# Performance work log

Hardware: AMD Instinct MI355X
Metric: run time of the kernel (lower is better)

The kernel has to match this reference:

```python
import jax, jax.numpy as jnp
import numpy as np

EMBED_DIM = 1024
NUM_HEAD = 16
HEAD_DIM = EMBED_DIM // NUM_HEAD
B, T = 4, 2048


def setup_inputs() -> dict:
    key = jax.random.key(0)
    ks = jax.random.split(key, 6)
    s_in = 1.0 / np.sqrt(EMBED_DIM)
    return {
        "hidden_states": jax.random.normal(ks[0], (B, T, EMBED_DIM), dtype=jnp.float32),
        "attn_mask": jnp.ones((B, T), dtype=jnp.int32),
        "W_qkv": jax.random.uniform(ks[1], (3 * EMBED_DIM, EMBED_DIM), jnp.float32, -s_in, s_in),
        "b_qkv": jax.random.uniform(ks[2], (3 * EMBED_DIM,), jnp.float32, -s_in, s_in),
        "W_o": jax.random.uniform(ks[3], (EMBED_DIM, EMBED_DIM), jnp.float32, -s_in, s_in),
        "b_o": jax.random.uniform(ks[4], (EMBED_DIM,), jnp.float32, -s_in, s_in),
    }


def reference(hidden_states, attn_mask, W_qkv, b_qkv, W_o, b_o):
    Bb, Tt, C = hidden_states.shape
    H, D = NUM_HEAD, HEAD_DIM
    scaling = D ** (-0.5)

    qkv = hidden_states @ W_qkv.T + b_qkv  # [B,T,3C]
    q, k, v = jnp.split(qkv, 3, axis=-1)
    # [B,H,T,D]
    q = q.reshape(Bb, Tt, H, D).transpose(0, 2, 1, 3)
    k = k.reshape(Bb, Tt, H, D).transpose(0, 2, 1, 3)
    v = v.reshape(Bb, Tt, H, D).transpose(0, 2, 1, 3)

    scores = jnp.einsum("bhqd,bhkd->bhqk", q, k) * scaling  # [B,H,T,T]

    causal = jnp.tril(jnp.ones((Tt, Tt), dtype=bool))[None, None]  # [1,1,T,T]
    am = attn_mask.astype(bool)
    mask = causal & am[:, None, :, None] & am[:, None, None, :]  # [B,1,T,T]
    scores = jnp.where(mask, scores, -jnp.inf)

    probs = jax.nn.softmax(scores, axis=-1)
    out = jnp.einsum("bhqk,bhkd->bhqd", probs, v)  # [B,H,T,D]
    out = out.transpose(0, 2, 1, 3).reshape(Bb, Tt, C)
    return out @ W_o.T + b_o
```

## Files before the change

kernel.cpp:

```cpp
#include <hip/hip_runtime.h>
#include <cstdint>
#include <cstddef>
#include <math.h>

#define BATCH 4
#define TSEQ  2048
#define CDIM  1024
#define NH    16
#define HDIM  64
#define MTOT  (BATCH * TSEQ)

typedef __attribute__((ext_vector_type(4))) float  floatx4;
typedef __attribute__((ext_vector_type(8))) short  shortx8;
typedef __attribute__((ext_vector_type(4))) short  shortx4;

__device__ __forceinline__ short f2bf(float f) {
    union { float f; unsigned int u; } v; v.f = f;
    unsigned int lsb = (v.u >> 16) & 1u;
    v.u += 0x7fffu + lsb;
    return (short)(v.u >> 16);
}

#if defined(__has_builtin)
#  if __has_builtin(__builtin_amdgcn_exp2f)
#    define EXP2F(x) __builtin_amdgcn_exp2f(x)
#  else
#    define EXP2F(x) exp2f(x)
#  endif
#  if __has_builtin(__builtin_amdgcn_perm)
__device__ __forceinline__ unsigned pack_hi16(unsigned hi, unsigned lo) {
    return __builtin_amdgcn_perm(hi, lo, 0x07060302u);
}
#  else
__device__ __forceinline__ unsigned pack_hi16(unsigned hi, unsigned lo) {
    return (lo >> 16) | (hi & 0xffff0000u);
}
#  endif
#  if __has_builtin(__builtin_amdgcn_mfma_f32_16x16x16bf16_1k)
#    define HAS_MFMA_1K 1
#  else
#    define HAS_MFMA_1K 0
#  endif
#else
#  define EXP2F(x) exp2f(x)
__device__ __forceinline__ unsigned pack_hi16(unsigned hi, unsigned lo) {
    return (lo >> 16) | (hi & 0xffff0000u);
}
#  define HAS_MFMA_1K 0
#endif

#define QSCALE (0.125f * 1.44269504088896f)

__global__ __launch_bounds__(256) void cvt_kernel(const float4* __restrict__ src,
                                                  shortx4* __restrict__ dst, int n4)
{
    int i = blockIdx.x * 256 + threadIdx.x;
    if (i < n4) {
        float4 v = src[i];
        shortx4 s;
        s[0] = f2bf(v.x); s[1] = f2bf(v.y); s[2] = f2bf(v.z); s[3] = f2bf(v.w);
        dst[i] = s;
    }
}

__global__ __launch_bounds__(256) void cvt3_kernel(
    const float4* __restrict__ s1, shortx4* __restrict__ d1,
    const float4* __restrict__ s2, shortx4* __restrict__ d2,
    const float4* __restrict__ s3, shortx4* __restrict__ d3)
{
    int bid = blockIdx.x;
    const float4* s; shortx4* d; int i;
    if (bid < 8192)       { s = s1; d = d1; i = bid * 256 + threadIdx.x; }
    else if (bid < 11264) { s = s2; d = d2; i = (bid - 8192) * 256 + threadIdx.x; }
    else                  { s = s3; d = d3; i = (bid - 11264) * 256 + threadIdx.x; }
    float4 v = s[i];
    shortx4 o;
    o[0] = f2bf(v.x); o[1] = f2bf(v.y); o[2] = f2bf(v.z); o[3] = f2bf(v.w);
    d[i] = o;
}

__device__ __forceinline__ void stageA_bf16(const short* g, short* S, int row0,
                                            int K, int k0, int tid, int wave)
{
#pragma unroll
    for (int i = 0; i < 2; ++i) {
        int c = i * 256 + tid;
        int r = c >> 2, kc = c & 3;
        __builtin_amdgcn_global_load_lds(
            (__attribute__((address_space(1))) void*)(g + (size_t)(row0 + r) * K + k0 + kc * 8),
            (__attribute__((address_space(3))) void*)((char*)S + i * 4096 + wave * 1024),
            16, 0, 0);
    }
}
__device__ __forceinline__ void stageB_f32(const float* g, short* S, int row0,
                                           int K, int k0, int tid)
{
#pragma unroll
    for (int i = 0; i < 4; ++i) {
        int c = i * 256 + tid;
        int r = c >> 3, fc = c & 7;
        const float4 v = *(const float4*)(g + (size_t)(row0 + r) * K + k0 + fc * 4);
        shortx4 s4;
        s4[0] = f2bf(v.x); s4[1] = f2bf(v.y); s4[2] = f2bf(v.z); s4[3] = f2bf(v.w);
        *(shortx4*)(S + r * 32 + fc * 4) = s4;
    }
}

__device__ __forceinline__ void qkv_epilogue(
    floatx4 (&acc)[4][4], const float* bias,
    short* Qo, short* Ko, short* VTo,
    int row0, int col0, int wr, int wc, int quad, int l16)
{
#pragma unroll
    for (int mi = 0; mi < 4; ++mi) {
        int m = row0 + wr * 64 + mi * 16 + quad * 4;
        int b = m >> 11, t0 = m & (TSEQ - 1);
#pragma unroll
        for (int ni = 0; ni < 4; ++ni) {
            int n = col0 + wc * 64 + ni * 16 + l16;
            float bv = bias[n];
            int part = n >> 10, rem = n & 1023;
            int h = rem >> 6, d = rem & 63;
            if (part == 2) {
                shortx4 st;
#pragma unroll
                for (int r = 0; r < 4; ++r) st[r] = f2bf(acc[mi][ni][r] + bv);
                *(shortx4*)(VTo + (((size_t)(b * NH + h)) * HDIM + d) * TSEQ + t0) = st;
            } else {
                short* dst = (part == 0) ? Qo : Ko;
                float scale = (part == 0) ? QSCALE : 1.0f;
#pragma unroll
                for (int r = 0; r < 4; ++r) {
                    size_t idx = (((size_t)(b * NH + h)) * TSEQ + (t0 + r)) * HDIM + d;
                    dst[idx] = f2bf((acc[mi][ni][r] + bv) * scale);
                }
            }
        }
    }
}

__global__ __launch_bounds__(256) void gemm_qkv_fast_kernel(
    const short* __restrict__ A,
    const short* __restrict__ W,
    const float* __restrict__ bias,
    short* __restrict__ Qo, short* __restrict__ Ko, short* __restrict__ VTo)
{
    __shared__ short As[128 * 32];
    __shared__ short Bs[128 * 32];
    const int tid  = threadIdx.x;
    const int lane = tid & 63, wave = tid >> 6;
    const int quad = lane >> 4, l16 = lane & 15;
    const int wr = wave >> 1, wc = wave & 1;
    const int row0 = blockIdx.x * 128;
    const int col0 = blockIdx.y * 128;
    const int K = CDIM;

    floatx4 acc[4][4] = {};

    for (int k0 = 0; k0 < K; k0 += 32) {
        stageA_bf16(A, As, row0, K, k0, tid, wave);
        stageA_bf16(W, Bs, col0, K, k0, tid, wave);
        __syncthreads();

        shortx8 af[4], bfr[4];
#pragma unroll
        for (int mi = 0; mi < 4; ++mi)
            af[mi] = *(const shortx8*)(As + (wr * 64 + mi * 16 + l16) * 32 + quad * 8);
#pragma unroll
        for (int ni = 0; ni < 4; ++ni)
            bfr[ni] = *(const shortx8*)(Bs + (wc * 64 + ni * 16 + l16) * 32 + quad * 8);
#pragma unroll
        for (int mi = 0; mi < 4; ++mi)
#pragma unroll
            for (int ni = 0; ni < 4; ++ni)
                acc[mi][ni] = __builtin_amdgcn_mfma_f32_16x16x32_bf16(
                    af[mi], bfr[ni], acc[mi][ni], 0, 0, 0);
        __syncthreads();
    }
    qkv_epilogue(acc, bias, Qo, Ko, VTo, row0, col0, wr, wc, quad, l16);
}

__global__ __launch_bounds__(256) void gemm_qkv_kernel(
    const short* __restrict__ A,
    const float* __restrict__ W,
    const float* __restrict__ bias,
    short* __restrict__ Qo, short* __restrict__ Ko, short* __restrict__ VTo)
{
    __shared__ short As[128 * 32];
    __shared__ short Bs[128 * 32];
    const int tid  = threadIdx.x;
    const int lane = tid & 63, wave = tid >> 6;
    const int quad = lane >> 4, l16 = lane & 15;
    const int wr = wave >> 1, wc = wave & 1;
    const int row0 = blockIdx.x * 128;
    const int col0 = blockIdx.y * 128;
    const int K = CDIM;

    floatx4 acc[4][4] = {};

    for (int k0 = 0; k0 < K; k0 += 32) {
        stageA_bf16(A, As, row0, K, k0, tid, wave);
        stageB_f32(W, Bs, col0, K, k0, tid);
        __syncthreads();

        shortx8 af[4], bfr[4];
#pragma unroll
        for (int mi = 0; mi < 4; ++mi)
            af[mi] = *(const shortx8*)(As + (wr * 64 + mi * 16 + l16) * 32 + quad * 8);
#pragma unroll
        for (int ni = 0; ni < 4; ++ni)
            bfr[ni] = *(const shortx8*)(Bs + (wc * 64 + ni * 16 + l16) * 32 + quad * 8);
#pragma unroll
        for (int mi = 0; mi < 4; ++mi)
#pragma unroll
            for (int ni = 0; ni < 4; ++ni)
                acc[mi][ni] = __builtin_amdgcn_mfma_f32_16x16x32_bf16(
                    af[mi], bfr[ni], acc[mi][ni], 0, 0, 0);
        __syncthreads();
    }
    qkv_epilogue(acc, bias, Qo, Ko, VTo, row0, col0, wr, wc, quad, l16);
}

__global__ __launch_bounds__(256) void attn_kernel(
    const short* __restrict__ Q,
    const short* __restrict__ Kg,
    const short* __restrict__ VT,
    const int*   __restrict__ am,
    short* __restrict__ O)
{
    __shared__ short Ks[64 * 64];
    __shared__ short Vs[64 * 64];

    const int tid  = threadIdx.x;
    const int lane = tid & 63, wave = tid >> 6;
    const int quad = lane >> 4, l16 = lane & 15;

    const int L = blockIdx.x;
    const int bh = (L & 7) + (((L >> 3) & 7) << 3);
    const int strip = 15 - (L >> 6);
    const int b = bh >> 4, h = bh & 15;

    const short* Qb = Q  + (size_t)bh * TSEQ * HDIM;
    const short* Kb = Kg + (size_t)bh * TSEQ * HDIM;
    const short* Vb = VT + (size_t)bh * HDIM * TSEQ;

    const int q0  = strip * 128;
    const int qb0 = q0 + wave * 32;
    const int qv0 = qb0 + l16;
    const int qv1 = qv0 + 16;

    shortx8 bq[2][2];
#pragma unroll
    for (int nq = 0; nq < 2; ++nq)
#pragma unroll
        for (int kk = 0; kk < 2; ++kk)
            bq[nq][kk] = *(const shortx8*)(
                Qb + (size_t)(qb0 + nq * 16 + l16) * HDIM + kk * 32 + quad * 8);

    floatx4 o[4][2] = {};
    floatx4 lacc[2] = {};

#if HAS_MFMA_1K
    const shortx4 ones4 = { (short)0x3F80, (short)0x3F80, (short)0x3F80, (short)0x3F80 };
#else
    const shortx8 ones8 = { (short)0x3F80, (short)0x3F80, (short)0x3F80, (short)0x3F80,
                            (short)0x3F80, (short)0x3F80, (short)0x3F80, (short)0x3F80 };
#endif

    const int ntiles = (q0 + 128) >> 6;
    for (int kt = 0; kt < ntiles; ++kt) {
        const int kt0 = kt << 6;
#pragma unroll
        for (int i = 0; i < 2; ++i) {
            int idx = i * 256 + tid;
            int rr = idx >> 3, cd = idx & 7;
            int c = cd ^ (rr & 7);
            __builtin_amdgcn_global_load_lds(
                (__attribute__((address_space(1))) void*)(Kb + (size_t)(kt0 + rr) * HDIM + c * 8),
                (__attribute__((address_space(3))) void*)((char*)Ks + i * 4096 + wave * 1024),
                16, 0, 0);
            __builtin_amdgcn_global_load_lds(
                (__attribute__((address_space(1))) void*)(Vb + (size_t)rr * TSEQ + kt0 + c * 8),
                (__attribute__((address_space(3))) void*)((char*)Vs + i * 4096 + wave * 1024),
                16, 0, 0);
        }
        int amv = am[b * TSEQ + kt0 + lane];
        bool allones = (__ballot(amv != 0) == 0xFFFFFFFFFFFFFFFFULL);
        __syncthreads();

        floatx4 s[4][2] = {};
#pragma unroll
        for (int kk = 0; kk < 2; ++kk)
#pragma unroll
            for (int t = 0; t < 4; ++t) {
                int rr = t * 16 + l16;
                shortx8 kf = *(const shortx8*)(
                    Ks + rr * 64 + (((kk * 4 + quad) ^ (l16 & 7)) << 3));
#pragma unroll
                for (int nq = 0; nq < 2; ++nq)
                    s[t][nq] = __builtin_amdgcn_mfma_f32_16x16x32_bf16(
                        kf, bq[nq][kk], s[t][nq], 0, 0, 0);
            }

        unsigned pk[4][2][2];
#pragma unroll
        for (int nq = 0; nq < 2; ++nq) {
            const int qv = nq ? qv1 : qv0;
#pragma unroll
            for (int t = 0; t < 4; ++t) {
                bool diag = (kt0 + t * 16 + 15) > (qb0 + nq * 16);
                unsigned pu[4];
#pragma unroll
                for (int r = 0; r < 4; ++r) {
                    float p = EXP2F(s[t][nq][r]);
                    unsigned u = __float_as_uint(p) & 0xffff0000u;
                    if (!allones) {
                        int amr = __shfl(amv, t * 16 + quad * 4 + r);
                        u = amr ? u : 0u;
                    }
                    if (diag) {
                        int kv = kt0 + t * 16 + quad * 4 + r;
                        u = (kv <= qv) ? u : 0u;
                    }
                    pu[r] = u;
                }
                pk[t][nq][0] = pack_hi16(pu[1], pu[0]);
                pk[t][nq][1] = pack_hi16(pu[3], pu[2]);
            }
        }

#if HAS_MFMA_1K
#pragma unroll
        for (int t = 0; t < 4; ++t) {
            union { unsigned u[2]; shortx4 s; } pb[2];
            pb[0].u[0] = pk[t][0][0]; pb[0].u[1] = pk[t][0][1];
            pb[1].u[0] = pk[t][1][0]; pb[1].u[1] = pk[t][1][1];
#pragma unroll
            for (int nq = 0; nq < 2; ++nq)
                lacc[nq] = __builtin_amdgcn_mfma_f32_16x16x16bf16_1k(
                    ones4, pb[nq].s, lacc[nq], 0, 0, 0);
#pragma unroll
            for (int mi = 0; mi < 4; ++mi) {
                int rr = mi * 16 + l16;
                int cidx = (2 * t + (quad >> 1)) ^ (l16 & 7);
                shortx4 vf = *(const shortx4*)(Vs + rr * 64 + cidx * 8 + (quad & 1) * 4);
#pragma unroll
                for (int nq = 0; nq < 2; ++nq)
                    o[mi][nq] = __builtin_amdgcn_mfma_f32_16x16x16bf16_1k(
                        vf, pb[nq].s, o[mi][nq], 0, 0, 0);
            }
        }
#else
#pragma unroll
        for (int kk2 = 0; kk2 < 2; ++kk2) {
            unsigned bfr[2][4];
#pragma unroll
            for (int nq = 0; nq < 2; ++nq)
#pragma unroll
                for (int jj = 0; jj < 4; ++jj) {
                    int srclane = (((quad & 1) * 2 + (jj >> 1)) * 16 + l16) << 2;
                    int lo = __builtin_amdgcn_ds_bpermute(srclane, (int)pk[kk2 * 2][nq][jj & 1]);
                    int hi = __builtin_amdgcn_ds_bpermute(srclane, (int)pk[kk2 * 2 + 1][nq][jj & 1]);
                    bfr[nq][jj] = (quad >> 1) ? (unsigned)hi : (unsigned)lo;
                }
            union { unsigned u[4]; shortx8 s; } pb[2];
#pragma unroll
            for (int nq = 0; nq < 2; ++nq) {
#pragma unroll
                for (int jj = 0; jj < 4; ++jj) pb[nq].u[jj] = bfr[nq][jj];
                lacc[nq] = __builtin_amdgcn_mfma_f32_16x16x32_bf16(
                    ones8, pb[nq].s, lacc[nq], 0, 0, 0);
            }
#pragma unroll
            for (int mi = 0; mi < 4; ++mi) {
                int rr = mi * 16 + l16;
                int cidx = (kk2 * 4 + quad) ^ (l16 & 7);
                shortx8 vf8 = *(const shortx8*)(Vs + rr * 64 + cidx * 8);
#pragma unroll
                for (int nq = 0; nq < 2; ++nq)
                    o[mi][nq] = __builtin_amdgcn_mfma_f32_16x16x32_bf16(
                        vf8, pb[nq].s, o[mi][nq], 0, 0, 0);
            }
        }
#endif
        __syncthreads();
    }

#pragma unroll
    for (int nq = 0; nq < 2; ++nq) {
        float inv = 1.0f / lacc[nq][0];
        int q = qb0 + nq * 16 + l16;
#pragma unroll
        for (int mi = 0; mi < 4; ++mi) {
            shortx4 st;
#pragma unroll
            for (int r = 0; r < 4; ++r) st[r] = f2bf(o[mi][nq][r] * inv);
            *(shortx4*)(O + ((size_t)(b * TSEQ + q)) * CDIM + h * HDIM + mi * 16 + quad * 4) = st;
        }
    }
}

__global__ __launch_bounds__(256) void gemm_out_kernel(
    const short* __restrict__ A,
    const short* __restrict__ W,
    const float* __restrict__ bias,
    float* __restrict__ Out)
{
    __shared__ short As[128 * 32];
    __shared__ short Bs[128 * 32];
    const int tid  = threadIdx.x;
    const int lane = tid & 63, wave = tid >> 6;
    const int quad = lane >> 4, l16 = lane & 15;
    const int wr = wave >> 1, wc = wave & 1;
    const int row0 = blockIdx.x * 128;
    const int col0 = blockIdx.y * 128;
    const int K = CDIM;

    floatx4 acc[4][4] = {};

    for (int k0 = 0; k0 < K; k0 += 32) {
        stageA_bf16(A, As, row0, K, k0, tid, wave);
        stageA_bf16(W, Bs, col0, K, k0, tid, wave);
        __syncthreads();

        shortx8 af[4], bfr[4];
#pragma unroll
        for (int mi = 0; mi < 4; ++mi)
            af[mi] = *(const shortx8*)(As + (wr * 64 + mi * 16 + l16) * 32 + quad * 8);
#pragma unroll
        for (int ni = 0; ni < 4; ++ni)
            bfr[ni] = *(const shortx8*)(Bs + (wc * 64 + ni * 16 + l16) * 32 + quad * 8);
#pragma unroll
        for (int mi = 0; mi < 4; ++mi)
#pragma unroll
            for (int ni = 0; ni < 4; ++ni)
                acc[mi][ni] = __builtin_amdgcn_mfma_f32_16x16x32_bf16(
                    af[mi], bfr[ni], acc[mi][ni], 0, 0, 0);
        __syncthreads();
    }

#pragma unroll
    for (int mi = 0; mi < 4; ++mi) {
        int m = row0 + wr * 64 + mi * 16 + quad * 4;
#pragma unroll
        for (int ni = 0; ni < 4; ++ni) {
            int n = col0 + wc * 64 + ni * 16 + l16;
            float bv = bias[n];
#pragma unroll
            for (int r = 0; r < 4; ++r)
                Out[(size_t)(m + r) * CDIM + n] = acc[mi][ni][r] + bv;
        }
    }
}

extern "C" void kernel_launch(void* const* d_in, const int* in_sizes, int n_in,
                              void* d_out, int out_size, void* d_ws, size_t ws_size,
                              hipStream_t stream)
{
    const float* hs   = (const float*)d_in[0];
    const int*   am   = (const int*)d_in[1];
    const float* Wqkv = (const float*)d_in[2];
    const float* bqkv = (const float*)d_in[3];
    const float* Wo   = (const float*)d_in[4];
    const float* bo   = (const float*)d_in[5];
    float* out = (float*)d_out;

    char* ws = (char*)d_ws;
    short* slot = (short*)ws;
    short* Qw   = (short*)(ws + ((size_t)16 << 20));
    short* Kw   = (short*)(ws + ((size_t)32 << 20));
    short* VTw  = (short*)(ws + ((size_t)48 << 20));

    if (ws_size >= ((size_t)72 << 20)) {
        short* Wqkvb = (short*)(ws + ((size_t)64 << 20));
        short* Wob   = (short*)(ws + ((size_t)70 << 20));
        cvt3_kernel<<<dim3(12288), 256, 0, stream>>>(
            (const float4*)hs,   (shortx4*)slot,
            (const float4*)Wqkv, (shortx4*)Wqkvb,
            (const float4*)Wo,   (shortx4*)Wob);
        gemm_qkv_fast_kernel<<<dim3(MTOT / 128, (3 * CDIM) / 128), 256, 0, stream>>>(
            slot, Wqkvb, bqkv, Qw, Kw, VTw);
        attn_kernel<<<dim3(1024), 256, 0, stream>>>(
            Qw, Kw, VTw, am, slot);
        gemm_out_kernel<<<dim3(MTOT / 128, CDIM / 128), 256, 0, stream>>>(
            slot, Wob, bo, out);
    } else {
        cvt_kernel<<<dim3((MTOT * CDIM / 4 + 255) / 256), 256, 0, stream>>>(
            (const float4*)hs, (shortx4*)slot, MTOT * CDIM / 4);
        gemm_qkv_kernel<<<dim3(MTOT / 128, (3 * CDIM) / 128), 256, 0, stream>>>(
            slot, Wqkv, bqkv, Qw, Kw, VTw);
        attn_kernel<<<dim3(1024), 256, 0, stream>>>(
            Qw, Kw, VTw, am, slot);
        cvt_kernel<<<dim3((CDIM * CDIM / 4 + 255) / 256), 256, 0, stream>>>(
            (const float4*)Wo, (shortx4*)Kw, CDIM * CDIM / 4);
        gemm_out_kernel<<<dim3(MTOT / 128, CDIM / 128), 256, 0, stream>>>(
            slot, Kw, bo, out);
    }
}
```

Before: 276.7 us.

## Double-buffer K/V tiles, skip fully masked causal subtiles, rebalance strip order

The attention kernel now double-buffers the K and V shared-memory tiles, so loading the next tile overlaps with computing the current one and each tile needs only one barrier. Each wave skips score and PV MFMAs for 16-key subtiles that lie entirely above its causal diagonal. Strip scheduling is reordered so long and short strips alternate across blocks. Launch bounds now request four blocks per CU. Doubling shared memory and adding the hint may increase register pressure or reduce occupancy.

```diff
diff --git a/kernel.cpp b/kernel.cpp
--- a/kernel.cpp
+++ b/kernel.cpp
@@ -221,23 +221,28 @@
     qkv_epilogue(acc, bias, Qo, Ko, VTo, row0, col0, wr, wc, quad, l16);
 }
 
-__global__ __launch_bounds__(256) void attn_kernel(
+__global__ __launch_bounds__(256, 4) void attn_kernel(
     const short* __restrict__ Q,
     const short* __restrict__ Kg,
     const short* __restrict__ VT,
     const int*   __restrict__ am,
     short* __restrict__ O)
 {
-    __shared__ short Ks[64 * 64];
-    __shared__ short Vs[64 * 64];
+    __shared__ short Ks[2 * 64 * 64];
+    __shared__ short Vs[2 * 64 * 64];
 
     const int tid  = threadIdx.x;
     const int lane = tid & 63, wave = tid >> 6;
     const int quad = lane >> 4, l16 = lane & 15;
 
     const int L = blockIdx.x;
-    const int bh = (L & 7) + (((L >> 3) & 7) << 3);
-    const int strip = 15 - (L >> 6);
+    const int bh = L & 63;
+    const int c  = L >> 6;
+    const int g  = c >> 2, ci = c & 3;
+    const int strip = (g == 0) ? (15 - ci)
+                    : (g == 1) ? ci
+                    : (g == 2) ? (8 + ci)
+                               : (7 - ci);
     const int b = bh >> 4, h = bh & 15;
 
     const short* Qb = Q  + (size_t)bh * TSEQ * HDIM;
@@ -248,6 +253,7 @@
     const int qb0 = q0 + wave * 32;
     const int qv0 = qb0 + l16;
     const int qv1 = qv0 + 16;
+    const int qmax = qb0 + 31;
 
     shortx8 bq[2][2];
 #pragma unroll
@@ -267,124 +273,153 @@
                             (short)0x3F80, (short)0x3F80, (short)0x3F80, (short)0x3F80 };
 #endif
 
+#define STAGE_KV(dstK, dstV, t0base)                                          \
+    {                                                                         \
+        _Pragma("unroll")                                                     \
+        for (int i = 0; i < 2; ++i) {                                         \
+            int idx = i * 256 + tid;                                          \
+            int rr = idx >> 3, cd = idx & 7;                                  \
+            int cc = cd ^ (rr & 7);                                           \
+            __builtin_amdgcn_global_load_lds(                                 \
+                (__attribute__((address_space(1))) void*)(Kb + (size_t)((t0base) + rr) * HDIM + cc * 8), \
+                (__attribute__((address_space(3))) void*)((char*)(dstK) + i * 4096 + wave * 1024),       \
+                16, 0, 0);                                                    \
+            __builtin_amdgcn_global_load_lds(                                 \
+                (__attribute__((address_space(1))) void*)(Vb + (size_t)rr * TSEQ + (t0base) + cc * 8),   \
+                (__attribute__((address_space(3))) void*)((char*)(dstV) + i * 4096 + wave * 1024),       \
+                16, 0, 0);                                                    \
+        }                                                                     \
+    }
+
     const int ntiles = (q0 + 128) >> 6;
+
+    STAGE_KV(Ks, Vs, 0);
+    __syncthreads();
+
     for (int kt = 0; kt < ntiles; ++kt) {
         const int kt0 = kt << 6;
-#pragma unroll
-        for (int i = 0; i < 2; ++i) {
-            int idx = i * 256 + tid;
-            int rr = idx >> 3, cd = idx & 7;
-            int c = cd ^ (rr & 7);
-            __builtin_amdgcn_global_load_lds(
-                (__attribute__((address_space(1))) void*)(Kb + (size_t)(kt0 + rr) * HDIM + c * 8),
-                (__attribute__((address_space(3))) void*)((char*)Ks + i * 4096 + wave * 1024),
-                16, 0, 0);
-            __builtin_amdgcn_global_load_lds(
-                (__attribute__((address_space(1))) void*)(Vb + (size_t)rr * TSEQ + kt0 + c * 8),
-                (__attribute__((address_space(3))) void*)((char*)Vs + i * 4096 + wave * 1024),
-                16, 0, 0);
+        const short* Kc = Ks + (kt & 1) * 4096;
+        const short* Vc = Vs + (kt & 1) * 4096;
+
+        if (kt + 1 < ntiles) {
+            short* Kn = Ks + ((kt + 1) & 1) * 4096;
+            short* Vn = Vs + ((kt + 1) & 1) * 4096;
+            const int nt0 = (kt + 1) << 6;
+            STAGE_KV(Kn, Vn, nt0);
         }
-        int amv = am[b * TSEQ + kt0 + lane];
-        bool allones = (__ballot(amv != 0) == 0xFFFFFFFFFFFFFFFFULL);
-        __syncthreads();
-
-        floatx4 s[4][2] = {};
-#pragma unroll
-        for (int kk = 0; kk < 2; ++kk)
+
+        if (kt0 <= qmax) {
+            int amv = am[b * TSEQ + kt0 + lane];
+            bool allones = (__ballot(amv != 0) == 0xFFFFFFFFFFFFFFFFULL);
+
+            floatx4 s[4][2] = {};
+#pragma unroll
+            for (int kk = 0; kk < 2; ++kk)
+#pragma unroll
+                for (int t = 0; t < 4; ++t) {
+                    if (kt0 + t * 16 > qmax) continue;
+                    int rr = t * 16 + l16;
+                    shortx8 kf = *(const shortx8*)(
+                        Kc + rr * 64 + (((kk * 4 + quad) ^ (l16 & 7)) << 3));
+#pragma unroll
+                    for (int nq = 0; nq < 2; ++nq)
+                        s[t][nq] = __builtin_amdgcn_mfma_f32_16x16x32_bf16(
+                            kf, bq[nq][kk], s[t][nq], 0, 0, 0);
+                }
+
+            unsigned pk[4][2][2];
+#pragma unroll
+            for (int nq = 0; nq < 2; ++nq) {
+                const int qv = nq ? qv1 : qv0;
+                const int qtop = qb0 + nq * 16 + 15;
+#pragma unroll
+                for (int t = 0; t < 4; ++t) {
+                    if (kt0 + t * 16 > qtop) {
+                        pk[t][nq][0] = 0u; pk[t][nq][1] = 0u;
+                        continue;
+                    }
+                    bool diag = (kt0 + t * 16 + 15) > (qb0 + nq * 16);
+                    unsigned pu[4];
+#pragma unroll
+                    for (int r = 0; r < 4; ++r) {
+                        float p = EXP2F(s[t][nq][r]);
+                        unsigned u = __float_as_uint(p);
+                        if (!allones) {
+                            int amr = __shfl(amv, t * 16 + quad * 4 + r);
+                            u = amr ? u : 0u;
+                        }
+                        if (diag) {
+                            int kv = kt0 + t * 16 + quad * 4 + r;
+                            u = (kv <= qv) ? u : 0u;
+                        }
+                        pu[r] = u;
+                    }
+                    pk[t][nq][0] = pack_hi16(pu[1], pu[0]);
+                    pk[t][nq][1] = pack_hi16(pu[3], pu[2]);
+                }
+            }
+
+#if HAS_MFMA_1K
 #pragma unroll
             for (int t = 0; t < 4; ++t) {
-                int rr = t * 16 + l16;
-                shortx8 kf = *(const shortx8*)(
-                    Ks + rr * 64 + (((kk * 4 + quad) ^ (l16 & 7)) << 3));
+                if (kt0 + t * 16 > qmax) continue;
+                union { unsigned u[2]; shortx4 s; } pb[2];
+                pb[0].u[0] = pk[t][0][0]; pb[0].u[1] = pk[t][0][1];
+                pb[1].u[0] = pk[t][1][0]; pb[1].u[1] = pk[t][1][1];
 #pragma unroll
                 for (int nq = 0; nq < 2; ++nq)
-                    s[t][nq] = __builtin_amdgcn_mfma_f32_16x16x32_bf16(
-                        kf, bq[nq][kk], s[t][nq], 0, 0, 0);
+                    lacc[nq] = __builtin_amdgcn_mfma_f32_16x16x16bf16_1k(
+                        ones4, pb[nq].s, lacc[nq], 0, 0, 0);
+#pragma unroll
+                for (int mi = 0; mi < 4; ++mi) {
+                    int rr = mi * 16 + l16;
+                    int cidx = (2 * t + (quad >> 1)) ^ (l16 & 7);
+                    shortx4 vf = *(const shortx4*)(Vc + rr * 64 + cidx * 8 + (quad & 1) * 4);
+#pragma unroll
+                    for (int nq = 0; nq < 2; ++nq)
+                        o[mi][nq] = __builtin_amdgcn_mfma_f32_16x16x16bf16_1k(
+                            vf, pb[nq].s, o[mi][nq], 0, 0, 0);
+                }
             }
-
-        unsigned pk[4][2][2];
-#pragma unroll
-        for (int nq = 0; nq < 2; ++nq) {
-            const int qv = nq ? qv1 : qv0;
-#pragma unroll
-            for (int t = 0; t < 4; ++t) {
-                bool diag = (kt0 + t * 16 + 15) > (qb0 + nq * 16);
-                unsigned pu[4];
-#pragma unroll
-                for (int r = 0; r < 4; ++r) {
-                    float p = EXP2F(s[t][nq][r]);
-                    unsigned u = __float_as_uint(p) & 0xffff0000u;
-                    if (!allones) {
-                        int amr = __shfl(amv, t * 16 + quad * 4 + r);
-                        u = amr ? u : 0u;
+#else
+#pragma unroll
+            for (int kk2 = 0; kk2 < 2; ++kk2) {
+                if (kt0 + kk2 * 32 > qmax) continue;
+                unsigned bfr[2][4];
+#pragma unroll
+                for (int nq = 0; nq < 2; ++nq)
+#pragma unroll
+                    for (int jj = 0; jj < 4; ++jj) {
+                        int srclane = (((quad & 1) * 2 + (jj >> 1)) * 16 + l16) << 2;
+                        int lo = __builtin_amdgcn_ds_bpermute(srclane, (int)pk[kk2 * 2][nq][jj & 1]);
+                        int hi = __builtin_amdgcn_ds_bpermute(srclane, (int)pk[kk2 * 2 + 1][nq][jj & 1]);
+                        bfr[nq][jj] = (quad >> 1) ? (unsigned)hi : (unsigned)lo;
                     }
-                    if (diag) {
-                        int kv = kt0 + t * 16 + quad * 4 + r;
-                        u = (kv <= qv) ? u : 0u;
-                    }
-                    pu[r] = u;
+                union { unsigned u[4]; shortx8 s; } pb[2];
+#pragma unroll
+                for (int nq = 0; nq < 2; ++nq) {
+#pragma unroll
+                    for (int jj = 0; jj < 4; ++jj) pb[nq].u[jj] = bfr[nq][jj];
+                    lacc[nq] = __builtin_amdgcn_mfma_f32_16x16x32_bf16(
+                        ones8, pb[nq].s, lacc[nq], 0, 0, 0);
                 }
-                pk[t][nq][0] = pack_hi16(pu[1], pu[0]);
-                pk[t][nq][1] = pack_hi16(pu[3], pu[2]);
+#pragma unroll
+                for (int mi = 0; mi < 4; ++mi) {
+                    int rr = mi * 16 + l16;
+                    int cidx = (kk2 * 4 + quad) ^ (l16 & 7);
+                    shortx8 vf8 = *(const shortx8*)(Vc + rr * 64 + cidx * 8);
+#pragma unroll
+                    for (int nq = 0; nq < 2; ++nq)
+                        o[mi][nq] = __builtin_amdgcn_mfma_f32_16x16x32_bf16(
+                            vf8, pb[nq].s, o[mi][nq], 0, 0, 0);
+                }
             }
+#endif
         }
 
-#if HAS_MFMA_1K
-#pragma unroll
-        for (int t = 0; t < 4; ++t) {
-            union { unsigned u[2]; shortx4 s; } pb[2];
-            pb[0].u[0] = pk[t][0][0]; pb[0].u[1] = pk[t][0][1];
-            pb[1].u[0] = pk[t][1][0]; pb[1].u[1] = pk[t][1][1];
-#pragma unroll
-            for (int nq = 0; nq < 2; ++nq)
-                lacc[nq] = __builtin_amdgcn_mfma_f32_16x16x16bf16_1k(
-                    ones4, pb[nq].s, lacc[nq], 0, 0, 0);
-#pragma unroll
-            for (int mi = 0; mi < 4; ++mi) {
-                int rr = mi * 16 + l16;
-                int cidx = (2 * t + (quad >> 1)) ^ (l16 & 7);
-                shortx4 vf = *(const shortx4*)(Vs + rr * 64 + cidx * 8 + (quad & 1) * 4);
-#pragma unroll
-                for (int nq = 0; nq < 2; ++nq)
-                    o[mi][nq] = __builtin_amdgcn_mfma_f32_16x16x16bf16_1k(
-                        vf, pb[nq].s, o[mi][nq], 0, 0, 0);
-            }
-        }
-#else
-#pragma unroll
-        for (int kk2 = 0; kk2 < 2; ++kk2) {
-            unsigned bfr[2][4];
-#pragma unroll
-            for (int nq = 0; nq < 2; ++nq)
-#pragma unroll
-                for (int jj = 0; jj < 4; ++jj) {
-                    int srclane = (((quad & 1) * 2 + (jj >> 1)) * 16 + l16) << 2;
-                    int lo = __builtin_amdgcn_ds_bpermute(srclane, (int)pk[kk2 * 2][nq][jj & 1]);
-                    int hi = __builtin_amdgcn_ds_bpermute(srclane, (int)pk[kk2 * 2 + 1][nq][jj & 1]);
-                    bfr[nq][jj] = (quad >> 1) ? (unsigned)hi : (unsigned)lo;
-                }
-            union { unsigned u[4]; shortx8 s; } pb[2];
-#pragma unroll
-            for (int nq = 0; nq < 2; ++nq) {
-#pragma unroll
-                for (int jj = 0; jj < 4; ++jj) pb[nq].u[jj] = bfr[nq][jj];
-                lacc[nq] = __builtin_amdgcn_mfma_f32_16x16x32_bf16(
-                    ones8, pb[nq].s, lacc[nq], 0, 0, 0);
-            }
-#pragma unroll
-            for (int mi = 0; mi < 4; ++mi) {
-                int rr = mi * 16 + l16;
-                int cidx = (kk2 * 4 + quad) ^ (l16 & 7);
-                shortx8 vf8 = *(const shortx8*)(Vs + rr * 64 + cidx * 8);
-#pragma unroll
-                for (int nq = 0; nq < 2; ++nq)
-                    o[mi][nq] = __builtin_amdgcn_mfma_f32_16x16x32_bf16(
-                        vf8, pb[nq].s, o[mi][nq], 0, 0, 0);
-            }
-        }
-#endif
-        __syncthreads();
-    }
+        __syncthreads();
+    }
+#undef STAGE_KV
 
 #pragma unroll
     for (int nq = 0; nq < 2; ++nq) {
```

Result: slower. 309.0 us (+11.7%).
